# Performance work log

Hardware: AMD Instinct MI355X
Metric: run time of the kernel (lower is better)

Reference implementation:

```python
import jax, jax.numpy as jnp
import numpy as np

EPS = 1e-5
BLOCK = 16

def setup_inputs() -> dict:
    key = jax.random.key(0)
    ks = jax.random.split(key, 5)
    B, S, D = 8, 4096, 1024
    G = D // BLOCK            # 64 groups
    sq = int(np.sqrt(D))      # 32
    x = jax.random.normal(ks[0], (B, S, D), dtype=jnp.float32)
    gamma = jnp.ones((D,), jnp.float32)
    beta = jnp.zeros((D,), jnp.float32)
    block_weights = 0.5 * jax.random.normal(ks[1], (G, BLOCK, BLOCK), dtype=jnp.float32)
    W_row = 0.1 * jax.random.normal(ks[2], (sq, sq), dtype=jnp.float32)
    W_col = 0.1 * jax.random.normal(ks[3], (sq, sq), dtype=jnp.float32)
    alpha = jnp.float32(0.3)
    bias = jnp.zeros((D,), jnp.float32)
    return {"x": x, "gamma": gamma, "beta": beta, "block_weights": block_weights,
            "W_row": W_row, "W_col": W_col, "alpha": alpha, "bias": bias}

def reference(x, gamma, beta, block_weights, W_row, W_col, alpha, bias):
    D = x.shape[-1]
    G, Bk, _ = block_weights.shape      # 64, 16, 16 (D == G*Bk, no pad)
    sq = W_row.shape[0]                 # 32 (D == sq*sq, no pad)
    # LayerNorm (fp32)
    mu = jnp.mean(x, axis=-1, keepdims=True)
    var = jnp.mean(jnp.square(x - mu), axis=-1, keepdims=True)
    xn = (x - mu) * jax.lax.rsqrt(var + EPS) * gamma + beta
    x_flat = xn.reshape(-1, D)          # [N, D]
    # Block-diagonal mix: [N, G, Bk] x [G, Bk, Bk]
    xg = x_flat.reshape(-1, G, Bk)
    y = jnp.einsum('ngb,gbc->ngc', xg, block_weights).reshape(-1, D)
    block_out = jnp.flip(y, axis=-1)
    # Monarch path: [N, sq, sq] @ W_col @ W_row^T
    xgrid = x_flat.reshape(-1, sq, sq)
    z = jnp.einsum('nrc,ck,sk->nrs', xgrid, W_col, W_row).reshape(-1, D)
    out = block_out + alpha * z + bias
    return out.reshape(x.shape)
```

## Files before the change

### kernel.cpp

```cpp
#include <hip/hip_runtime.h>

typedef __bf16 bf16x8 __attribute__((ext_vector_type(8)));
typedef __bf16 bf16x4 __attribute__((ext_vector_type(4)));
typedef float f32x4 __attribute__((ext_vector_type(4)));

#define EPS 1e-5f

__global__ __launch_bounds__(256) void hbsl_precompute(
    const float* __restrict__ bw, const float* __restrict__ W_row,
    const float* __restrict__ W_col, const float* __restrict__ alpha_p,
    __bf16* __restrict__ mt, __bf16* __restrict__ bwt)
{
    const int t = threadIdx.x;
    if (blockIdx.x == 0) {
        const float alpha = alpha_p[0];
        #pragma unroll
        for (int k = 0; k < 4; ++k) {
            int flat = t + 256 * k;
            int s = flat >> 5, c = flat & 31;
            float acc = 0.f;
            #pragma unroll 8
            for (int kk = 0; kk < 32; ++kk)
                acc += W_col[c * 32 + kk] * W_row[s * 32 + kk];
            mt[s * 32 + c] = (__bf16)(alpha * acc);
        }
    } else {
        int g = blockIdx.x - 1;
        int c = t >> 4, b = t & 15;
        bwt[g * 256 + c * 16 + b] = (__bf16)bw[g * 256 + b * 16 + c];
    }
}

__global__ __launch_bounds__(256, 4) void hbsl_main(
    const float* __restrict__ x, const float* __restrict__ gamma,
    const float* __restrict__ beta, const float* __restrict__ bias,
    const __bf16* __restrict__ mt, const __bf16* __restrict__ bwt,
    float* __restrict__ out)
{
    __shared__ __bf16 xn[16 * 1032];
    __shared__ float bias_s[1024];
    const int t = threadIdx.x;
    const int lane = t & 63;
    const int wv = t >> 6;
    const int q = lane >> 4, n = lane & 15;
    const int row = t >> 4, li = t & 15;
    const int rbase = blockIdx.x * 16;

    bf16x8 mfrag0 = *(const bf16x8*)(mt + n * 32 + q * 8);
    bf16x8 mfrag1 = *(const bf16x8*)(mt + (16 + n) * 32 + q * 8);

    bf16x8 bwf[8];
    #pragma unroll
    for (int p = 0; p < 8; ++p) {
        const int o0 = wv * 16 + 2 * p;
        const int gp = 31 - (o0 >> 1);
        const int g = (q >= 2) ? (2 * gp + 1) : (2 * gp);
        const int e = (q >= 2) ? (q - 2) * 8 : q * 8;
        bwf[p] = *(const bf16x8*)(bwt + g * 256 + (15 - n) * 16 + e);
    }

    *(float4*)(&bias_s[t * 4]) = *(const float4*)(bias + t * 4);

    const float* xr = x + (size_t)(rbase + row) * 1024;
    float4 xv[16];
    float s = 0.f, ss = 0.f;
    #pragma unroll
    for (int i = 0; i < 16; ++i) {
        xv[i] = *(const float4*)(xr + li * 4 + i * 64);
        s += xv[i].x + xv[i].y + xv[i].z + xv[i].w;
        ss += xv[i].x * xv[i].x + xv[i].y * xv[i].y
            + xv[i].z * xv[i].z + xv[i].w * xv[i].w;
    }
    #pragma unroll
    for (int m = 1; m < 16; m <<= 1) {
        s  += __shfl_xor(s, m, 64);
        ss += __shfl_xor(ss, m, 64);
    }
    const float mu = s * (1.f / 1024.f);
    const float rstd = rsqrtf(ss * (1.f / 1024.f) - mu * mu + EPS);
    #pragma unroll
    for (int i = 0; i < 16; ++i) {
        const int col = li * 4 + i * 64;
        float4 g4 = *(const float4*)(gamma + col);
        float4 b4 = *(const float4*)(beta + col);
        bf16x4 v;
        v[0] = (__bf16)((xv[i].x - mu) * rstd * g4.x + b4.x);
        v[1] = (__bf16)((xv[i].y - mu) * rstd * g4.y + b4.y);
        v[2] = (__bf16)((xv[i].z - mu) * rstd * g4.z + b4.z);
        v[3] = (__bf16)((xv[i].w - mu) * rstd * g4.w + b4.w);
        *(bf16x4*)(&xn[row * 1032 + col]) = v;
    }
    __syncthreads();

    bf16x8 bz;
    #pragma unroll
    for (int i = 0; i < 8; ++i) bz[i] = (__bf16)0.f;
    const f32x4 zf = {0.f, 0.f, 0.f, 0.f};

    #pragma unroll
    for (int p = 0; p < 8; ++p) {
        const int o0 = wv * 16 + 2 * p;
        const int r  = o0 >> 1;
        const int gp = 31 - r;

        bf16x8 az = *(const bf16x8*)(&xn[n * 1032 + r  * 32 + q * 8]);
        bf16x8 ay = *(const bf16x8*)(&xn[n * 1032 + gp * 32 + q * 8]);

        bf16x8 a0 = (q >= 2) ? bwf[p] : bz;
        bf16x8 a1 = (q <  2) ? bwf[p] : bz;

        f32x4 z0 = __builtin_amdgcn_mfma_f32_16x16x32_bf16(mfrag0, az, zf, 0, 0, 0);
        f32x4 z1 = __builtin_amdgcn_mfma_f32_16x16x32_bf16(mfrag1, az, zf, 0, 0, 0);
        f32x4 y0 = __builtin_amdgcn_mfma_f32_16x16x32_bf16(a0, ay, zf, 0, 0, 0);
        f32x4 y1 = __builtin_amdgcn_mfma_f32_16x16x32_bf16(a1, ay, zf, 0, 0, 0);

        f32x4 b0 = *(const f32x4*)(&bias_s[o0 * 16 + q * 4]);
        f32x4 b1 = *(const f32x4*)(&bias_s[o0 * 16 + 16 + q * 4]);

        float* op = out + (size_t)(rbase + n) * 1024 + o0 * 16 + q * 4;
        *(f32x4*)op        = y0 + z0 + b0;
        *(f32x4*)(op + 16) = y1 + z1 + b1;
    }
}

extern "C" void kernel_launch(void* const* d_in, const int* in_sizes, int n_in,
                              void* d_out, int out_size, void* d_ws, size_t ws_size,
                              hipStream_t stream) {
    const float* x      = (const float*)d_in[0];
    const float* gamma  = (const float*)d_in[1];
    const float* beta   = (const float*)d_in[2];
    const float* bw     = (const float*)d_in[3];
    const float* W_row  = (const float*)d_in[4];
    const float* W_col  = (const float*)d_in[5];
    const float* alpha  = (const float*)d_in[6];
    const float* bias   = (const float*)d_in[7];
    float* o = (float*)d_out;

    __bf16* mt  = (__bf16*)d_ws;
    __bf16* bwt = (__bf16*)((char*)d_ws + 2048);

    const int N = in_sizes[0] / 1024;

    hipLaunchKernelGGL(hbsl_precompute, dim3(65), dim3(256), 0, stream,
                       bw, W_row, W_col, alpha, mt, bwt);
    hipLaunchKernelGGL(hbsl_main, dim3(N / 16), dim3(256), 0, stream,
                       x, gamma, beta, bias, mt, bwt, o);
}
```

Before: 259.2 us.

## Use 512-thread blocks with wave-per-row LayerNorm, swizzled LDS, and chained MFMA accumulation

```diff
diff --git a/kernel.cpp b/kernel.cpp
--- a/kernel.cpp
+++ b/kernel.cpp
@@ -9,14 +9,14 @@
 __global__ __launch_bounds__(256) void hbsl_precompute(
     const float* __restrict__ bw, const float* __restrict__ W_row,
     const float* __restrict__ W_col, const float* __restrict__ alpha_p,
-    __bf16* __restrict__ mt, __bf16* __restrict__ bwt)
+    __bf16* __restrict__ mt, __bf16* __restrict__ bwt2)
 {
     const int t = threadIdx.x;
     if (blockIdx.x == 0) {
         const float alpha = alpha_p[0];
         #pragma unroll
-        for (int k = 0; k < 4; ++k) {
-            int flat = t + 256 * k;
+        for (int k4 = 0; k4 < 4; ++k4) {
+            int flat = t + 256 * k4;
             int s = flat >> 5, c = flat & 31;
             float acc = 0.f;
             #pragma unroll 8
@@ -25,101 +25,96 @@
             mt[s * 32 + c] = (__bf16)(alpha * acc);
         }
     } else {
-        int g = blockIdx.x - 1;
-        int c = t >> 4, b = t & 15;
-        bwt[g * 256 + c * 16 + b] = (__bf16)bw[g * 256 + b * 16 + c];
+        const int o = blockIdx.x - 1;
+        const int g = 63 - o;
+        #pragma unroll
+        for (int hh = 0; hh < 2; ++hh) {
+            const int idx = t + hh * 256;
+            const int m = idx >> 5, k = idx & 31;
+            float v = 0.f;
+            if ((k >> 4) != (o & 1))
+                v = bw[g * 256 + (k & 15) * 16 + (15 - m)];
+            bwt2[o * 512 + idx] = (__bf16)v;
+        }
     }
 }
 
-__global__ __launch_bounds__(256, 4) void hbsl_main(
+__global__ __launch_bounds__(512, 8) void hbsl_main(
     const float* __restrict__ x, const float* __restrict__ gamma,
     const float* __restrict__ beta, const float* __restrict__ bias,
-    const __bf16* __restrict__ mt, const __bf16* __restrict__ bwt,
+    const __bf16* __restrict__ mt, const __bf16* __restrict__ bwt2,
     float* __restrict__ out)
 {
-    __shared__ __bf16 xn[16 * 1032];
-    __shared__ float bias_s[1024];
+    __shared__ __bf16 xn[16 * 1024];
     const int t = threadIdx.x;
     const int lane = t & 63;
     const int wv = t >> 6;
     const int q = lane >> 4, n = lane & 15;
-    const int row = t >> 4, li = t & 15;
     const int rbase = blockIdx.x * 16;
 
-    bf16x8 mfrag0 = *(const bf16x8*)(mt + n * 32 + q * 8);
-    bf16x8 mfrag1 = *(const bf16x8*)(mt + (16 + n) * 32 + q * 8);
-
-    bf16x8 bwf[8];
     #pragma unroll
-    for (int p = 0; p < 8; ++p) {
-        const int o0 = wv * 16 + 2 * p;
-        const int gp = 31 - (o0 >> 1);
-        const int g = (q >= 2) ? (2 * gp + 1) : (2 * gp);
-        const int e = (q >= 2) ? (q - 2) * 8 : q * 8;
-        bwf[p] = *(const bf16x8*)(bwt + g * 256 + (15 - n) * 16 + e);
+    for (int it = 0; it < 2; ++it) {
+        const int r = it * 8 + wv;
+        const float* xr = x + (size_t)(rbase + r) * 1024 + lane * 4;
+        float4 v0 = *(const float4*)(xr);
+        float4 v1 = *(const float4*)(xr + 256);
+        float4 v2 = *(const float4*)(xr + 512);
+        float4 v3 = *(const float4*)(xr + 768);
+        float s  = (v0.x + v0.y + v0.z + v0.w) + (v1.x + v1.y + v1.z + v1.w)
+                 + (v2.x + v2.y + v2.z + v2.w) + (v3.x + v3.y + v3.z + v3.w);
+        float ss = (v0.x*v0.x + v0.y*v0.y + v0.z*v0.z + v0.w*v0.w)
+                 + (v1.x*v1.x + v1.y*v1.y + v1.z*v1.z + v1.w*v1.w)
+                 + (v2.x*v2.x + v2.y*v2.y + v2.z*v2.z + v2.w*v2.w)
+                 + (v3.x*v3.x + v3.y*v3.y + v3.z*v3.z + v3.w*v3.w);
+        #pragma unroll
+        for (int msk = 1; msk < 64; msk <<= 1) {
+            s  += __shfl_xor(s,  msk, 64);
+            ss += __shfl_xor(ss, msk, 64);
+        }
+        const float mu   = s * (1.f / 1024.f);
+        const float rstd = rsqrtf(ss * (1.f / 1024.f) - mu * mu + EPS);
+        const int base = r * 1024;
+        const int swz  = (r & 7) << 3;
+        #pragma unroll
+        for (int j = 0; j < 4; ++j) {
+            const float4 v = (j == 0) ? v0 : (j == 1) ? v1 : (j == 2) ? v2 : v3;
+            const int col = lane * 4 + j * 256;
+            const float4 g4 = *(const float4*)(gamma + col);
+            const float4 b4 = *(const float4*)(beta + col);
+            bf16x4 w;
+            w[0] = (__bf16)((v.x - mu) * rstd * g4.x + b4.x);
+            w[1] = (__bf16)((v.y - mu) * rstd * g4.y + b4.y);
+            w[2] = (__bf16)((v.z - mu) * rstd * g4.z + b4.z);
+            w[3] = (__bf16)((v.w - mu) * rstd * g4.w + b4.w);
+            *(bf16x4*)(&xn[base + (col ^ swz)]) = w;
+        }
     }
 
-    *(float4*)(&bias_s[t * 4]) = *(const float4*)(bias + t * 4);
+    const bf16x8 mfrag0 = *(const bf16x8*)(mt + n * 32 + q * 8);
+    const bf16x8 mfrag1 = *(const bf16x8*)(mt + (16 + n) * 32 + q * 8);
 
-    const float* xr = x + (size_t)(rbase + row) * 1024;
-    float4 xv[16];
-    float s = 0.f, ss = 0.f;
-    #pragma unroll
-    for (int i = 0; i < 16; ++i) {
-        xv[i] = *(const float4*)(xr + li * 4 + i * 64);
-        s += xv[i].x + xv[i].y + xv[i].z + xv[i].w;
-        ss += xv[i].x * xv[i].x + xv[i].y * xv[i].y
-            + xv[i].z * xv[i].z + xv[i].w * xv[i].w;
-    }
-    #pragma unroll
-    for (int m = 1; m < 16; m <<= 1) {
-        s  += __shfl_xor(s, m, 64);
-        ss += __shfl_xor(ss, m, 64);
-    }
-    const float mu = s * (1.f / 1024.f);
-    const float rstd = rsqrtf(ss * (1.f / 1024.f) - mu * mu + EPS);
-    #pragma unroll
-    for (int i = 0; i < 16; ++i) {
-        const int col = li * 4 + i * 64;
-        float4 g4 = *(const float4*)(gamma + col);
-        float4 b4 = *(const float4*)(beta + col);
-        bf16x4 v;
-        v[0] = (__bf16)((xv[i].x - mu) * rstd * g4.x + b4.x);
-        v[1] = (__bf16)((xv[i].y - mu) * rstd * g4.y + b4.y);
-        v[2] = (__bf16)((xv[i].z - mu) * rstd * g4.z + b4.z);
-        v[3] = (__bf16)((xv[i].w - mu) * rstd * g4.w + b4.w);
-        *(bf16x4*)(&xn[row * 1032 + col]) = v;
-    }
     __syncthreads();
 
-    bf16x8 bz;
+    const int rswz = (n & 7) << 3;
+    float* orow = out + (size_t)(rbase + n) * 1024;
     #pragma unroll
-    for (int i = 0; i < 8; ++i) bz[i] = (__bf16)0.f;
-    const f32x4 zf = {0.f, 0.f, 0.f, 0.f};
-
-    #pragma unroll
-    for (int p = 0; p < 8; ++p) {
-        const int o0 = wv * 16 + 2 * p;
+    for (int p = 0; p < 4; ++p) {
+        const int o0 = wv * 8 + 2 * p;
         const int r  = o0 >> 1;
         const int gp = 31 - r;
-
-        bf16x8 az = *(const bf16x8*)(&xn[n * 1032 + r  * 32 + q * 8]);
-        bf16x8 ay = *(const bf16x8*)(&xn[n * 1032 + gp * 32 + q * 8]);
-
-        bf16x8 a0 = (q >= 2) ? bwf[p] : bz;
-        bf16x8 a1 = (q <  2) ? bwf[p] : bz;
-
-        f32x4 z0 = __builtin_amdgcn_mfma_f32_16x16x32_bf16(mfrag0, az, zf, 0, 0, 0);
-        f32x4 z1 = __builtin_amdgcn_mfma_f32_16x16x32_bf16(mfrag1, az, zf, 0, 0, 0);
-        f32x4 y0 = __builtin_amdgcn_mfma_f32_16x16x32_bf16(a0, ay, zf, 0, 0, 0);
-        f32x4 y1 = __builtin_amdgcn_mfma_f32_16x16x32_bf16(a1, ay, zf, 0, 0, 0);
-
-        f32x4 b0 = *(const f32x4*)(&bias_s[o0 * 16 + q * 4]);
-        f32x4 b1 = *(const f32x4*)(&bias_s[o0 * 16 + 16 + q * 4]);
-
-        float* op = out + (size_t)(rbase + n) * 1024 + o0 * 16 + q * 4;
-        *(f32x4*)op        = y0 + z0 + b0;
-        *(f32x4*)(op + 16) = y1 + z1 + b1;
+        bf16x8 az = *(const bf16x8*)(&xn[n * 1024 + ((r  * 32 + q * 8) ^ rswz)]);
+        bf16x8 ay = *(const bf16x8*)(&xn[n * 1024 + ((gp * 32 + q * 8) ^ rswz)]);
+        bf16x8 a0 = *(const bf16x8*)(bwt2 + (o0    ) * 512 + n * 32 + q * 8);
+        bf16x8 a1 = *(const bf16x8*)(bwt2 + (o0 + 1) * 512 + n * 32 + q * 8);
+        f32x4 b0 = *(const f32x4*)(bias + o0 * 16 + q * 4);
+        f32x4 b1 = *(const f32x4*)(bias + o0 * 16 + 16 + q * 4);
+        f32x4 r0 = __builtin_amdgcn_mfma_f32_16x16x32_bf16(mfrag0, az, b0, 0, 0, 0);
+        f32x4 r1 = __builtin_amdgcn_mfma_f32_16x16x32_bf16(mfrag1, az, b1, 0, 0, 0);
+        r0 = __builtin_amdgcn_mfma_f32_16x16x32_bf16(a0, ay, r0, 0, 0, 0);
+        r1 = __builtin_amdgcn_mfma_f32_16x16x32_bf16(a1, ay, r1, 0, 0, 0);
+        float* op = orow + o0 * 16 + q * 4;
+        __builtin_nontemporal_store(r0, (f32x4*)op);
+        __builtin_nontemporal_store(r1, (f32x4*)(op + 16));
     }
 }
 
@@ -136,13 +131,13 @@
     const float* bias   = (const float*)d_in[7];
     float* o = (float*)d_out;
 
-    __bf16* mt  = (__bf16*)d_ws;
-    __bf16* bwt = (__bf16*)((char*)d_ws + 2048);
+    __bf16* mt   = (__bf16*)d_ws;
+    __bf16* bwt2 = (__bf16*)((char*)d_ws + 2048);
 
     const int N = in_sizes[0] / 1024;
 
     hipLaunchKernelGGL(hbsl_precompute, dim3(65), dim3(256), 0, stream,
-                       bw, W_row, W_col, alpha, mt, bwt);
-    hipLaunchKernelGGL(hbsl_main, dim3(N / 16), dim3(256), 0, stream,
-                       x, gamma, beta, bias, mt, bwt, o);
+                       bw, W_row, W_col, alpha, mt, bwt2);
+    hipLaunchKernelGGL(hbsl_main, dim3(N / 16), dim3(512), 0, stream,
+                       x, gamma, beta, bias, mt, bwt2, o);
 }
```

After: 270.5 us. 1.04x slower.

## Loop over multiple row tiles per block with register prefetch and swizzled LDS

Applied to the files above, without the earlier changes.

```diff
diff --git a/kernel.cpp b/kernel.cpp
--- a/kernel.cpp
+++ b/kernel.cpp
@@ -5,6 +5,7 @@
 typedef float f32x4 __attribute__((ext_vector_type(4)));
 
 #define EPS 1e-5f
+#define TPB_TILES 4
 
 __global__ __launch_bounds__(256) void hbsl_precompute(
     const float* __restrict__ bw, const float* __restrict__ W_row,
@@ -31,95 +32,129 @@
     }
 }
 
-__global__ __launch_bounds__(256, 4) void hbsl_main(
+__global__ __launch_bounds__(512, 4) void hbsl_main(
     const float* __restrict__ x, const float* __restrict__ gamma,
     const float* __restrict__ beta, const float* __restrict__ bias,
     const __bf16* __restrict__ mt, const __bf16* __restrict__ bwt,
     float* __restrict__ out)
 {
-    __shared__ __bf16 xn[16 * 1032];
+    __shared__ __bf16 xn[16 * 1024];
     __shared__ float bias_s[1024];
     const int t = threadIdx.x;
     const int lane = t & 63;
     const int wv = t >> 6;
     const int q = lane >> 4, n = lane & 15;
-    const int row = t >> 4, li = t & 15;
-    const int rbase = blockIdx.x * 16;
 
-    bf16x8 mfrag0 = *(const bf16x8*)(mt + n * 32 + q * 8);
-    bf16x8 mfrag1 = *(const bf16x8*)(mt + (16 + n) * 32 + q * 8);
-
-    bf16x8 bwf[8];
+    const bf16x8 mfrag0 = *(const bf16x8*)(mt + n * 32 + q * 8);
+    const bf16x8 mfrag1 = *(const bf16x8*)(mt + (16 + n) * 32 + q * 8);
+    bf16x8 bwf[4];
     #pragma unroll
-    for (int p = 0; p < 8; ++p) {
-        const int o0 = wv * 16 + 2 * p;
+    for (int p = 0; p < 4; ++p) {
+        const int o0 = wv * 8 + 2 * p;
         const int gp = 31 - (o0 >> 1);
         const int g = (q >= 2) ? (2 * gp + 1) : (2 * gp);
         const int e = (q >= 2) ? (q - 2) * 8 : q * 8;
         bwf[p] = *(const bf16x8*)(bwt + g * 256 + (15 - n) * 16 + e);
     }
-
-    *(float4*)(&bias_s[t * 4]) = *(const float4*)(bias + t * 4);
-
-    const float* xr = x + (size_t)(rbase + row) * 1024;
-    float4 xv[16];
-    float s = 0.f, ss = 0.f;
-    #pragma unroll
-    for (int i = 0; i < 16; ++i) {
-        xv[i] = *(const float4*)(xr + li * 4 + i * 64);
-        s += xv[i].x + xv[i].y + xv[i].z + xv[i].w;
-        ss += xv[i].x * xv[i].x + xv[i].y * xv[i].y
-            + xv[i].z * xv[i].z + xv[i].w * xv[i].w;
-    }
-    #pragma unroll
-    for (int m = 1; m < 16; m <<= 1) {
-        s  += __shfl_xor(s, m, 64);
-        ss += __shfl_xor(ss, m, 64);
-    }
-    const float mu = s * (1.f / 1024.f);
-    const float rstd = rsqrtf(ss * (1.f / 1024.f) - mu * mu + EPS);
-    #pragma unroll
-    for (int i = 0; i < 16; ++i) {
-        const int col = li * 4 + i * 64;
-        float4 g4 = *(const float4*)(gamma + col);
-        float4 b4 = *(const float4*)(beta + col);
-        bf16x4 v;
-        v[0] = (__bf16)((xv[i].x - mu) * rstd * g4.x + b4.x);
-        v[1] = (__bf16)((xv[i].y - mu) * rstd * g4.y + b4.y);
-        v[2] = (__bf16)((xv[i].z - mu) * rstd * g4.z + b4.z);
-        v[3] = (__bf16)((xv[i].w - mu) * rstd * g4.w + b4.w);
-        *(bf16x4*)(&xn[row * 1032 + col]) = v;
-    }
-    __syncthreads();
+    *(float2*)(&bias_s[t * 2]) = *(const float2*)(bias + t * 2);
 
     bf16x8 bz;
     #pragma unroll
     for (int i = 0; i < 8; ++i) bz[i] = (__bf16)0.f;
-    const f32x4 zf = {0.f, 0.f, 0.f, 0.f};
+
+    const int r0 = wv * 2, r1 = wv * 2 + 1;
+    const int wswz0 = (r0 & 7) << 3, wswz1 = (r1 & 7) << 3;
+    const int rswz  = (n & 7) << 3;
+    const int tile0 = blockIdx.x * TPB_TILES;
+
+    float4 va[4], vb[4];
+    {
+        const float* xr0 = x + (size_t)(tile0 * 16 + r0) * 1024 + lane * 4;
+        const float* xr1 = x + (size_t)(tile0 * 16 + r1) * 1024 + lane * 4;
+        #pragma unroll
+        for (int j = 0; j < 4; ++j) {
+            va[j] = *(const float4*)(xr0 + j * 256);
+            vb[j] = *(const float4*)(xr1 + j * 256);
+        }
+    }
 
     #pragma unroll
-    for (int p = 0; p < 8; ++p) {
-        const int o0 = wv * 16 + 2 * p;
-        const int r  = o0 >> 1;
-        const int gp = 31 - r;
+    for (int tt = 0; tt < TPB_TILES; ++tt) {
+        const int rbase = (tile0 + tt) * 16;
 
-        bf16x8 az = *(const bf16x8*)(&xn[n * 1032 + r  * 32 + q * 8]);
-        bf16x8 ay = *(const bf16x8*)(&xn[n * 1032 + gp * 32 + q * 8]);
+        float s0 = 0.f, q0 = 0.f, s1 = 0.f, q1 = 0.f;
+        #pragma unroll
+        for (int j = 0; j < 4; ++j) {
+            s0 += va[j].x + va[j].y + va[j].z + va[j].w;
+            q0 += va[j].x * va[j].x + va[j].y * va[j].y
+                + va[j].z * va[j].z + va[j].w * va[j].w;
+            s1 += vb[j].x + vb[j].y + vb[j].z + vb[j].w;
+            q1 += vb[j].x * vb[j].x + vb[j].y * vb[j].y
+                + vb[j].z * vb[j].z + vb[j].w * vb[j].w;
+        }
+        #pragma unroll
+        for (int m = 1; m < 64; m <<= 1) {
+            s0 += __shfl_xor(s0, m, 64);
+            q0 += __shfl_xor(q0, m, 64);
+            s1 += __shfl_xor(s1, m, 64);
+            q1 += __shfl_xor(q1, m, 64);
+        }
+        const float mu0 = s0 * (1.f / 1024.f);
+        const float rs0 = rsqrtf(q0 * (1.f / 1024.f) - mu0 * mu0 + EPS);
+        const float mu1 = s1 * (1.f / 1024.f);
+        const float rs1 = rsqrtf(q1 * (1.f / 1024.f) - mu1 * mu1 + EPS);
+        #pragma unroll
+        for (int j = 0; j < 4; ++j) {
+            const int col = lane * 4 + j * 256;
+            const float4 g4 = *(const float4*)(gamma + col);
+            const float4 b4 = *(const float4*)(beta + col);
+            bf16x4 w0, w1;
+            w0[0] = (__bf16)((va[j].x - mu0) * rs0 * g4.x + b4.x);
+            w0[1] = (__bf16)((va[j].y - mu0) * rs0 * g4.y + b4.y);
+            w0[2] = (__bf16)((va[j].z - mu0) * rs0 * g4.z + b4.z);
+            w0[3] = (__bf16)((va[j].w - mu0) * rs0 * g4.w + b4.w);
+            w1[0] = (__bf16)((vb[j].x - mu1) * rs1 * g4.x + b4.x);
+            w1[1] = (__bf16)((vb[j].y - mu1) * rs1 * g4.y + b4.y);
+            w1[2] = (__bf16)((vb[j].z - mu1) * rs1 * g4.z + b4.z);
+            w1[3] = (__bf16)((vb[j].w - mu1) * rs1 * g4.w + b4.w);
+            *(bf16x4*)(&xn[r0 * 1024 + (col ^ wswz0)]) = w0;
+            *(bf16x4*)(&xn[r1 * 1024 + (col ^ wswz1)]) = w1;
+        }
 
-        bf16x8 a0 = (q >= 2) ? bwf[p] : bz;
-        bf16x8 a1 = (q <  2) ? bwf[p] : bz;
+        __syncthreads();
 
-        f32x4 z0 = __builtin_amdgcn_mfma_f32_16x16x32_bf16(mfrag0, az, zf, 0, 0, 0);
-        f32x4 z1 = __builtin_amdgcn_mfma_f32_16x16x32_bf16(mfrag1, az, zf, 0, 0, 0);
-        f32x4 y0 = __builtin_amdgcn_mfma_f32_16x16x32_bf16(a0, ay, zf, 0, 0, 0);
-        f32x4 y1 = __builtin_amdgcn_mfma_f32_16x16x32_bf16(a1, ay, zf, 0, 0, 0);
+        if (tt + 1 < TPB_TILES) {
+            const float* nx0 = x + (size_t)(rbase + 16 + r0) * 1024 + lane * 4;
+            const float* nx1 = x + (size_t)(rbase + 16 + r1) * 1024 + lane * 4;
+            #pragma unroll
+            for (int j = 0; j < 4; ++j) {
+                va[j] = *(const float4*)(nx0 + j * 256);
+                vb[j] = *(const float4*)(nx1 + j * 256);
+            }
+        }
 
-        f32x4 b0 = *(const f32x4*)(&bias_s[o0 * 16 + q * 4]);
-        f32x4 b1 = *(const f32x4*)(&bias_s[o0 * 16 + 16 + q * 4]);
+        float* orow = out + (size_t)(rbase + n) * 1024;
+        #pragma unroll
+        for (int p = 0; p < 4; ++p) {
+            const int o0 = wv * 8 + 2 * p;
+            const int r  = o0 >> 1;
+            const int gp = 31 - r;
+            bf16x8 az = *(const bf16x8*)(&xn[n * 1024 + ((r  * 32 + q * 8) ^ rswz)]);
+            bf16x8 ay = *(const bf16x8*)(&xn[n * 1024 + ((gp * 32 + q * 8) ^ rswz)]);
+            bf16x8 a0 = (q >= 2) ? bwf[p] : bz;
+            bf16x8 a1 = (q <  2) ? bwf[p] : bz;
+            f32x4 b0 = *(const f32x4*)(&bias_s[o0 * 16 + q * 4]);
+            f32x4 b1 = *(const f32x4*)(&bias_s[o0 * 16 + 16 + q * 4]);
+            f32x4 d0 = __builtin_amdgcn_mfma_f32_16x16x32_bf16(mfrag0, az, b0, 0, 0, 0);
+            f32x4 d1 = __builtin_amdgcn_mfma_f32_16x16x32_bf16(mfrag1, az, b1, 0, 0, 0);
+            d0 = __builtin_amdgcn_mfma_f32_16x16x32_bf16(a0, ay, d0, 0, 0, 0);
+            d1 = __builtin_amdgcn_mfma_f32_16x16x32_bf16(a1, ay, d1, 0, 0, 0);
+            float* op = orow + o0 * 16 + q * 4;
+            *(f32x4*)op        = d0;
+            *(f32x4*)(op + 16) = d1;
+        }
 
-        float* op = out + (size_t)(rbase + n) * 1024 + o0 * 16 + q * 4;
-        *(f32x4*)op        = y0 + z0 + b0;
-        *(f32x4*)(op + 16) = y1 + z1 + b1;
+        if (tt + 1 < TPB_TILES) __syncthreads();
     }
 }
 
@@ -140,9 +175,10 @@
     __bf16* bwt = (__bf16*)((char*)d_ws + 2048);
 
     const int N = in_sizes[0] / 1024;
+    const int n_tiles = N / 16;
 
     hipLaunchKernelGGL(hbsl_precompute, dim3(65), dim3(256), 0, stream,
                        bw, W_row, W_col, alpha, mt, bwt);
-    hipLaunchKernelGGL(hbsl_main, dim3(N / 16), dim3(256), 0, stream,
+    hipLaunchKernelGGL(hbsl_main, dim3(n_tiles / TPB_TILES), dim3(512), 0, stream,
                        x, gamma, beta, bias, mt, bwt, o);
 }
```

After: 296.6 us. 1.14x slower.
